# Optimization experiments

Measured on AMD Instinct MI355X. Metric: run time of the kernel, lower is better.

## Reference

```python
import jax, jax.numpy as jnp
import numpy as np

B, F, Hh, Ww, C = 1, 8, 12, 18, 1920
HEADS, HD, RANK, TXT = 30, 64, 128, 224
VID = F * Hh * Ww  # 1728
DN = ('NCH', 'OIH', 'NCH')


def setup_inputs() -> dict:
    key = jax.random.key(0)
    ks = jax.random.split(key, 14)
    s = 0.02
    return {
        'hidden_states': jax.random.normal(ks[0], (B, VID, C), jnp.float32),
        'encoder_hidden_states': jax.random.normal(ks[1], (B, TXT, C), jnp.float32),
        'cos': jax.random.uniform(ks[2], (VID, HD), jnp.float32),
        'sin': jax.random.uniform(ks[3], (VID, HD), jnp.float32),
        'conv1_w': jax.random.normal(ks[4], (RANK, C, 3), jnp.float32) * s,
        'conv2_w': jax.random.normal(ks[5], (C, RANK, 3), jnp.float32) * s,
        'Wq': jax.random.normal(ks[6], (C, C), jnp.float32) * s,
        'bq': jnp.zeros((C,), jnp.float32),
        'Wk': jax.random.normal(ks[7], (C, C), jnp.float32) * s,
        'bk': jnp.zeros((C,), jnp.float32),
        'Wv': jax.random.normal(ks[8], (C, C), jnp.float32) * s,
        'bv': jnp.zeros((C,), jnp.float32),
        'Wo': jax.random.normal(ks[9], (C, C), jnp.float32) * s,
        'bo': jnp.zeros((C,), jnp.float32),
    }


def _rope(x, cos, sin):
    # x: [B, H, S_vid, D]; cos/sin: [S_vid, D]; interleaved rotate-half
    xr = x.reshape(*x.shape[:-1], -1, 2)
    x_rot = jnp.stack([-xr[..., 1], xr[..., 0]], axis=-1).reshape(x.shape)
    return x * cos + x_rot * sin


def reference(hidden_states, encoder_hidden_states, cos, sin, conv1_w, conv2_w,
              Wq, bq, Wk, bk, Wv, bv, Wo, bo):
    # temporal conv1d skip branch over frame axis per spatial location
    x = hidden_states.reshape(B, F, Hh, Ww, C).transpose(0, 2, 3, 4, 1)
    x = x.reshape(B * Hh * Ww, C, F)
    h = jax.lax.conv_general_dilated(x, conv1_w, (1,), [(1, 1)], dimension_numbers=DN)
    h = jax.nn.gelu(h, approximate=False)
    h = jax.lax.conv_general_dilated(h, conv2_w, (1,), [(1, 1)], dimension_numbers=DN)
    skip = h.reshape(B, Hh, Ww, C, F).transpose(0, 4, 1, 2, 3).reshape(B, VID, C)

    hs = jnp.concatenate([encoder_hidden_states, hidden_states + skip], axis=1)  # [B,S,C]

    q = (hs @ Wq.T + bq).reshape(B, -1, HEADS, HD).transpose(0, 2, 1, 3)
    k = (hs @ Wk.T + bk).reshape(B, -1, HEADS, HD).transpose(0, 2, 1, 3)
    v = (hs @ Wv.T + bv).reshape(B, -1, HEADS, HD).transpose(0, 2, 1, 3)

    # RoPE applied only to the video (image) tokens of q and k
    q = jnp.concatenate([q[:, :, :TXT], _rope(q[:, :, TXT:], cos, sin)], axis=2)
    k = jnp.concatenate([k[:, :, :TXT], _rope(k[:, :, TXT:], cos, sin)], axis=2)

    scores = jnp.einsum('bhqd,bhkd->bhqk', q, k) * (HD ** -0.5)
    attn = jax.nn.softmax(scores, axis=-1)
    o = jnp.einsum('bhqk,bhkd->bhqd', attn, v)
    o = o.transpose(0, 2, 1, 3).reshape(B, -1, HEADS * HD)
    o = o @ Wo.T + bo  # to_out[0]; to_out[1] is dropout (identity at eval)

    return (o[:, TXT:], o[:, :TXT])  # (hidden_states, encoder_hidden_states)
```

## Files before the change

### kernel.cpp

```cpp
#include <hip/hip_runtime.h>
#include <math.h>

typedef unsigned short u16;
typedef short short8 __attribute__((ext_vector_type(8)));
typedef short shortv4 __attribute__((ext_vector_type(4)));
typedef float f32x4 __attribute__((ext_vector_type(4)));

#define TXT 224
#define VID 1728
#define S_ALL 1952
#define C_DIM 1920
#define HD 64
#define RANK 128
#define SHD 124928

#define OFF_HS   ((size_t)0)
#define OFF_XPAD ((size_t)3932160)
#define OFF_O    OFF_XPAD
#define OFF_HG   ((size_t)8355840)
#define OFF_W1T  ((size_t)8650752)
#define OFF_W2T  ((size_t)9388032)
#define OFF_WQ   ((size_t)10125312)
#define OFF_WK   ((size_t)13811712)
#define OFF_WV   ((size_t)17498112)
#define OFF_WO   ((size_t)21184512)
#define OFF_Q    ((size_t)24870912)
#define OFF_K    ((size_t)28618752)
#define OFF_V    ((size_t)32366592)

__device__ __forceinline__ float b2f(u16 u) {
  union { unsigned int i; float f; } x; x.i = ((unsigned int)u) << 16; return x.f;
}
__device__ __forceinline__ u16 f2b(float f) {
  union { float f; unsigned int i; } x; x.f = f;
  unsigned int i = x.i;
  return (u16)((i + 0x7FFFu + ((i >> 16) & 1u)) >> 16);
}
__device__ __forceinline__ void gload16(const u16* g, short* l) {
  __builtin_amdgcn_global_load_lds((const __attribute__((address_space(1))) unsigned int*)g,
                                   (__attribute__((address_space(3))) unsigned int*)l, 16, 0, 0);
}

__global__ void __launch_bounds__(256) prep_kernel(const float* __restrict__ hidden,
                                                   const float* __restrict__ enc,
                                                   const float* __restrict__ w1,
                                                   const float* __restrict__ w2,
                                                   const float* __restrict__ Wq,
                                                   const float* __restrict__ Wk,
                                                   const float* __restrict__ Wv,
                                                   const float* __restrict__ Wo,
                                                   u16* __restrict__ ws) {
  size_t i = (size_t)blockIdx.x * 256 + threadIdx.x;
  if (i < 1105920) {
    const size_t e = i * 4;
    const int row = (int)(e / 1920), col = (int)(e % 1920);
    shortv4 o4 = {0, 0, 0, 0};
    if (row >= 216 && row < 1944) {
      const float4 f = *(const float4*)(hidden + (size_t)(row - 216) * 1920 + col);
      o4 = (shortv4){(short)f2b(f.x), (short)f2b(f.y), (short)f2b(f.z), (short)f2b(f.w)};
    }
    *(shortv4*)(ws + OFF_XPAD + e) = o4;
    return;
  }
  i -= 1105920;
  if (i < 184320) {
    const size_t e = i * 4;
    const int r = (int)(e / 5760), j = (int)(e % 5760), t = j / 1920, c = j % 1920;
    const float* s = w1 + (size_t)r * 5760 + (size_t)c * 3 + t;
    shortv4 o4 = {(short)f2b(s[0]), (short)f2b(s[3]), (short)f2b(s[6]), (short)f2b(s[9])};
    *(shortv4*)(ws + OFF_W1T + e) = o4;
    return;
  }
  i -= 184320;
  if (i < 184320) {
    const size_t e = i * 4;
    const int c = (int)(e / 384), j = (int)(e % 384), t = j / 128, r = j % 128;
    const float* s = w2 + (size_t)c * 384 + (size_t)r * 3 + t;
    shortv4 o4 = {(short)f2b(s[0]), (short)f2b(s[3]), (short)f2b(s[6]), (short)f2b(s[9])};
    *(shortv4*)(ws + OFF_W2T + e) = o4;
    return;
  }
  i -= 184320;
  if (i < 107520) {
    const size_t e = i * 4;
    const float4 f = *(const float4*)(enc + e);
    *(shortv4*)(ws + OFF_HS + e) =
        (shortv4){(short)f2b(f.x), (short)f2b(f.y), (short)f2b(f.z), (short)f2b(f.w)};
    return;
  }
  i -= 107520;
  if (i < 3686400) {
    const int j = (int)(i / 921600);
    const size_t e = (i - (size_t)j * 921600) * 4;
    const float* src = (j == 0) ? Wq : ((j == 1) ? Wk : ((j == 2) ? Wv : Wo));
    const float4 f = *(const float4*)(src + e);
    *(shortv4*)(ws + OFF_WQ + (size_t)j * 3686400 + e) =
        (shortv4){(short)f2b(f.x), (short)f2b(f.y), (short)f2b(f.z), (short)f2b(f.w)};
    return;
  }
  i -= 3686400;
  const short8 z8 = {0, 0, 0, 0, 0, 0, 0, 0};
  size_t e;
  if (i < 23040) e = OFF_HS + 3747840 + i * 8;
  else if (i < 26496) e = OFF_HG + (i - 23040) * 8;
  else if (i < 32256) e = OFF_HG + 248832 + (i - 26496) * 8;
  else e = OFF_O + 3747840 + (i - 32256) * 8;
  *(short8*)(ws + e) = z8;
}

struct GArgs {
  const u16 *A, *B0, *B1, *B2;
  const float *bias0, *bias1, *bias2;
  const float *cosp, *sinp, *hidden;
  u16 *out0, *out1, *out2;
  float* outf;
  int lda, ldb, ksteps, spt, tap_rows, nMt, nNt, Mvalid;
};

template <int BM, int BN, int EPI>
__global__ void __launch_bounds__(256) gemm_bt(GArgs a) {
  constexpr int WM = BM / 2, WN = BN / 2, FM = WM / 16, FN = WN / 16;
  __shared__ __align__(16) short lA[2][BM * 32];
  __shared__ __align__(16) short lB[2][BN * 32];
  const int tid = threadIdx.x;
  const int lane = tid & 63;
  const int wv = tid >> 6, wr = wv >> 1, wc = wv & 1;
  const int lr = lane & 15, lg = lane >> 4;
  const int mtile = blockIdx.x % a.nMt;
  const int ntile_raw = blockIdx.x / a.nMt;
  const int ntile = ntile_raw % a.nNt;
  const int slice = ntile_raw / a.nNt;
  const int kstart = slice * a.ksteps;
  const int sec = (ntile * BN) / C_DIM;
  const u16* Bw = (sec == 0) ? a.B0 : ((sec == 1) ? a.B1 : a.B2);
  const int nb = ntile * BN - sec * C_DIM;
  const int m0 = mtile * BM;

  f32x4 acc[FM][FN];
#pragma unroll
  for (int i = 0; i < FM; ++i)
#pragma unroll
    for (int j = 0; j < FN; ++j) acc[i][j] = (f32x4){0.f, 0.f, 0.f, 0.f};

  auto stageStep = [&](int buf, int gs) {
    const int tap = gs / a.spt;
    const int kcol = (gs - tap * a.spt) * 32;
    const int arow0 = m0 + tap * a.tap_rows;
#pragma unroll
    for (int i = 0; i < BM / 64; ++i) {
      const int o = (i * 256 + tid) * 16;
      const int row = o >> 6;
      const int ke = (o & 63) >> 1;
      gload16(a.A + (size_t)(arow0 + row) * a.lda + (kcol + ke), &lA[buf][o >> 1]);
    }
#pragma unroll
    for (int i = 0; i < BN / 64; ++i) {
      const int o = (i * 256 + tid) * 16;
      const int row = o >> 6;
      const int ke = (o & 63) >> 1;
      gload16(Bw + (size_t)(nb + row) * a.ldb + (gs * 32 + ke), &lB[buf][o >> 1]);
    }
  };

  stageStep(0, kstart);
  __syncthreads();
  int cur = 0;
  for (int s = 0; s < a.ksteps; ++s) {
    if (s + 1 < a.ksteps) stageStep(cur ^ 1, kstart + s + 1);
    short8 af[FM], bfr[FN];
#pragma unroll
    for (int i = 0; i < FM; ++i)
      af[i] = *(const short8*)(&lA[cur][(wr * WM + i * 16 + lr) * 32 + lg * 8]);
#pragma unroll
    for (int j = 0; j < FN; ++j)
      bfr[j] = *(const short8*)(&lB[cur][(wc * WN + j * 16 + lr) * 32 + lg * 8]);
#pragma unroll
    for (int i = 0; i < FM; ++i)
#pragma unroll
      for (int j = 0; j < FN; ++j)
        acc[i][j] = __builtin_amdgcn_mfma_f32_16x16x32_bf16(af[i], bfr[j], acc[i][j], 0, 0, 0);
    __syncthreads();
    cur ^= 1;
  }

#pragma unroll
  for (int i = 0; i < FM; ++i) {
#pragma unroll
    for (int j = 0; j < FN; ++j) {
      const int col = ntile * BN + wc * WN + j * 16 + lr;
#pragma unroll
      for (int r = 0; r < 4; ++r) {
        const int m = m0 + wr * WM + i * 16 + lg * 4 + r;
        float v = acc[i][j][r];
        if (EPI == 4) {
          if (m < a.Mvalid) a.outf[(size_t)slice * 221184 + (size_t)m * RANK + col] = v;
        } else if (EPI == 1) {
          if (m < a.Mvalid) {
            v += a.hidden[(size_t)m * C_DIM + col];
            a.out0[(size_t)m * C_DIM + col] = f2b(v);
          }
        } else if (EPI == 2) {
          const int nn = col - sec * C_DIM;
          const int hh = nn >> 6, d = nn & 63;
          const float* bias = (sec == 0) ? a.bias0 : ((sec == 1) ? a.bias1 : a.bias2);
          v += bias[nn];
          const float vp = __shfl_xor(v, 1);
          if (sec < 2 && m >= TXT) {
            const int vid = ((m < S_ALL) ? m : TXT) - TXT;
            const float c = a.cosp[vid * HD + d];
            const float sn = a.sinp[vid * HD + d];
            v = (d & 1) ? (v * c + vp * sn) : (v * c - vp * sn);
          }
          if (sec == 0) v *= 0.18033688011112042f;
          if (m < a.Mvalid) {
            u16* dst = (sec == 0) ? a.out0 : ((sec == 1) ? a.out1 : a.out2);
            dst[(size_t)hh * SHD + (size_t)m * HD + d] = f2b(v);
          }
        } else {
          v += a.bias0[col];
          if (m < a.Mvalid) {
            const int dr = (m >= TXT) ? (m - TXT) : (VID + m);
            a.outf[(size_t)dr * C_DIM + col] = v;
          }
        }
      }
    }
  }
}

__global__ void __launch_bounds__(256) c1reduce_kernel(const float* __restrict__ part,
                                                       u16* __restrict__ hg) {
  const int i = blockIdx.x * 256 + threadIdx.x;
  float s = 0.f;
#pragma unroll
  for (int j = 0; j < 6; ++j) s += part[(size_t)j * 221184 + i];
  const float g = 0.5f * s * (1.0f + erff(s * 0.70710678f));
  hg[i] = f2b(g);
}

__global__ void __launch_bounds__(256) vtrans_kernel(const u16* __restrict__ vin,
                                                     u16* __restrict__ vout) {
  __shared__ u16 t[64][72];
  const int b = blockIdx.x, hh = b / 31, mt = b % 31;
  const int m0 = mt * 64;
  const int rows = (m0 + 64 <= S_ALL) ? 64 : (S_ALL - m0);
  const int tid = threadIdx.x;
  const u16* src = vin + (size_t)hh * SHD + (size_t)m0 * HD;
#pragma unroll
  for (int p = 0; p < 2; ++p) {
    const int r = p * 32 + (tid >> 3), c = (tid & 7) * 8;
    short8 v8 = {0, 0, 0, 0, 0, 0, 0, 0};
    if (r < rows) v8 = *(const short8*)(src + (size_t)r * HD + c);
    *(short8*)&t[r][c] = v8;
  }
  __syncthreads();
  const int d = tid & 63, ms = tid >> 6;
  if (ms * 16 < rows) {
    short8 a0, a1;
#pragma unroll
    for (int x = 0; x < 8; ++x) { a0[x] = (short)t[ms * 16 + x][d]; a1[x] = (short)t[ms * 16 + 8 + x][d]; }
    u16* dst = vout + (size_t)hh * SHD + (size_t)d * S_ALL + m0 + ms * 16;
    *(short8*)dst = a0;
    *(short8*)(dst + 8) = a1;
  }
}

__global__ void __launch_bounds__(256) attn_kernel(const u16* __restrict__ q,
                                                   const u16* __restrict__ k,
                                                   const u16* __restrict__ vT,
                                                   u16* __restrict__ o) {
  __shared__ __align__(16) short lK[2][4096];
  __shared__ __align__(16) short lp[4][1024];
  const int bid = blockIdx.x;
  const int hh = bid / 31, qt = bid - hh * 31;
  const int tid = threadIdx.x, wv = tid >> 6, lane = tid & 63;
  const int lr = lane & 15, lg = lane >> 4;
  const int qbase = qt * 64 + wv * 16;
  const bool active = qbase < S_ALL;
  const u16* qh = q + (size_t)hh * SHD;
  const u16* kh = k + (size_t)hh * SHD;
  const u16* vh = vT + (size_t)hh * SHD;

  int krow[2], kcol[2], kdst[2];
#pragma unroll
  for (int j = 0; j < 2; ++j) {
    const int p0 = (j * 256 + tid) * 8;
    const int row = p0 >> 6, cs = p0 & 63;
    kdst[j] = p0;
    krow[j] = row;
    kcol[j] = cs ^ ((row & 7) * 8);
  }

  short8 aq0 = {}, aq1 = {};
  if (active) {
    aq0 = *(const short8*)(qh + (size_t)(qbase + lr) * HD + lg * 8);
    aq1 = *(const short8*)(qh + (size_t)(qbase + lr) * HD + 32 + lg * 8);
  }
  f32x4 oa[4];
#pragma unroll
  for (int gd = 0; gd < 4; ++gd) oa[gd] = (f32x4){0.f, 0.f, 0.f, 0.f};
  float mr = -3.0e38f, lw = 0.f;
  const f32x4 z4 = (f32x4){0.f, 0.f, 0.f, 0.f};
  const int pmask = (lr & 7) * 8;
  short* lpw = &lp[wv][0];
  const u16* vrow[4];
#pragma unroll
  for (int gd = 0; gd < 4; ++gd) vrow[gd] = vh + (size_t)(gd * 16 + lr) * S_ALL + lg * 8;

#pragma unroll
  for (int j = 0; j < 2; ++j) gload16(kh + (size_t)krow[j] * HD + kcol[j], &lK[0][kdst[j]]);
  __syncthreads();

  int cur = 0;
  for (int t = 0; t < 30; ++t) {
    const int kb = t * 64;
    if (t < 29) {
#pragma unroll
      for (int j = 0; j < 2; ++j)
        gload16(kh + (size_t)(kb + 64 + krow[j]) * HD + kcol[j], &lK[cur ^ 1][kdst[j]]);
    }
    if (active) {
      const short* Kt = &lK[cur][0];
      f32x4 st[4];
      __builtin_amdgcn_s_setprio(1);
#pragma unroll
      for (int k16 = 0; k16 < 4; ++k16) {
        const int row = k16 * 16 + lr;
        const int m8 = (row & 7) * 8;
        short8 kf0 = *(const short8*)(Kt + row * 64 + ((lg * 8) ^ m8));
        short8 kf1 = *(const short8*)(Kt + row * 64 + ((32 + lg * 8) ^ m8));
        st[k16] = __builtin_amdgcn_mfma_f32_16x16x32_bf16(kf0, aq0, z4, 0, 0, 0);
        st[k16] = __builtin_amdgcn_mfma_f32_16x16x32_bf16(kf1, aq1, st[k16], 0, 0, 0);
      }
      __builtin_amdgcn_s_setprio(0);
      short8 vf[4][2];
#pragma unroll
      for (int gd = 0; gd < 4; ++gd) {
        vf[gd][0] = *(const short8*)(vrow[gd] + kb);
        vf[gd][1] = *(const short8*)(vrow[gd] + kb + 32);
      }
      float tm = fmaxf(fmaxf(fmaxf(st[0][0], st[0][1]), fmaxf(st[0][2], st[0][3])),
                       fmaxf(fmaxf(st[1][0], st[1][1]), fmaxf(st[1][2], st[1][3])));
      tm = fmaxf(tm, fmaxf(fmaxf(fmaxf(st[2][0], st[2][1]), fmaxf(st[2][2], st[2][3])),
                           fmaxf(fmaxf(st[3][0], st[3][1]), fmaxf(st[3][2], st[3][3]))));
      tm = fmaxf(tm, __shfl_xor(tm, 16));
      tm = fmaxf(tm, __shfl_xor(tm, 32));
      const bool defer = (__all(tm <= mr + 8.0f) != 0);
      float al = 1.0f;
      if (!defer) {
        const float mn = fmaxf(mr, tm);
        al = __builtin_exp2f(mr - mn);
        mr = mn;
      }
      float rs = 0.f;
#pragma unroll
      for (int k16 = 0; k16 < 4; ++k16) {
        float p0 = __builtin_exp2f(st[k16][0] - mr);
        float p1 = __builtin_exp2f(st[k16][1] - mr);
        float p2 = __builtin_exp2f(st[k16][2] - mr);
        float p3 = __builtin_exp2f(st[k16][3] - mr);
        rs += (p0 + p1) + (p2 + p3);
        uint2 pk;
        asm("v_cvt_pk_bf16_f32 %0, %1, %2" : "=v"(pk.x) : "v"(p0), "v"(p1));
        asm("v_cvt_pk_bf16_f32 %0, %1, %2" : "=v"(pk.y) : "v"(p2), "v"(p3));
        *(uint2*)(lpw + lr * 64 + ((k16 * 16 + lg * 4) ^ pmask)) = pk;
      }
      rs += __shfl_xor(rs, 16);
      rs += __shfl_xor(rs, 32);
      lw = lw * al + rs;
      asm volatile("s_waitcnt lgkmcnt(0)" ::: "memory");
      short8 pa0 = *(const short8*)(lpw + lr * 64 + ((lg * 8) ^ pmask));
      short8 pa1 = *(const short8*)(lpw + lr * 64 + ((32 + lg * 8) ^ pmask));
      float alp[4];
      if (!defer) {
#pragma unroll
        for (int r = 0; r < 4; ++r) alp[r] = __shfl(al, lg * 4 + r);
      }
      __builtin_amdgcn_s_setprio(1);
#pragma unroll
      for (int gd = 0; gd < 4; ++gd) {
        f32x4 tacc = oa[gd];
        if (!defer) {
#pragma unroll
          for (int r = 0; r < 4; ++r) tacc[r] *= alp[r];
        }
        tacc = __builtin_amdgcn_mfma_f32_16x16x32_bf16(pa0, vf[gd][0], tacc, 0, 0, 0);
        oa[gd] = __builtin_amdgcn_mfma_f32_16x16x32_bf16(pa1, vf[gd][1], tacc, 0, 0, 0);
      }
      __builtin_amdgcn_s_setprio(0);
    }
    __syncthreads();
    cur ^= 1;
  }

  if (active) {
    const u16* kp = kh + (size_t)1920 * HD + (size_t)lr * HD + lg * 8;
    short8 kf00 = *(const short8*)(kp);
    short8 kf01 = *(const short8*)(kp + 32);
    short8 kf10 = *(const short8*)(kp + 16 * HD);
    short8 kf11 = *(const short8*)(kp + 16 * HD + 32);
    f32x4 st0 = __builtin_amdgcn_mfma_f32_16x16x32_bf16(kf00, aq0, z4, 0, 0, 0);
    st0 = __builtin_amdgcn_mfma_f32_16x16x32_bf16(kf01, aq1, st0, 0, 0, 0);
    f32x4 st1 = __builtin_amdgcn_mfma_f32_16x16x32_bf16(kf10, aq0, z4, 0, 0, 0);
    st1 = __builtin_amdgcn_mfma_f32_16x16x32_bf16(kf11, aq1, st1, 0, 0, 0);
    float tm = fmaxf(fmaxf(fmaxf(st0[0], st0[1]), fmaxf(st0[2], st0[3])),
                     fmaxf(fmaxf(st1[0], st1[1]), fmaxf(st1[2], st1[3])));
    tm = fmaxf(tm, __shfl_xor(tm, 16));
    tm = fmaxf(tm, __shfl_xor(tm, 32));
    const float mn = fmaxf(mr, tm);
    const float al = __builtin_exp2f(mr - mn);
    mr = mn;
    float rs = 0.f;
    float pp[8];
#pragma unroll
    for (int r = 0; r < 4; ++r) { pp[r] = __builtin_exp2f(st0[r] - mn); rs += pp[r]; }
#pragma unroll
    for (int r = 0; r < 4; ++r) { pp[4 + r] = __builtin_exp2f(st1[r] - mn); rs += pp[4 + r]; }
    {
      uint2 pk;
      asm("v_cvt_pk_bf16_f32 %0, %1, %2" : "=v"(pk.x) : "v"(pp[0]), "v"(pp[1]));
      asm("v_cvt_pk_bf16_f32 %0, %1, %2" : "=v"(pk.y) : "v"(pp[2]), "v"(pp[3]));
      *(uint2*)(lpw + lr * 64 + ((lg * 4) ^ pmask)) = pk;
      asm("v_cvt_pk_bf16_f32 %0, %1, %2" : "=v"(pk.x) : "v"(pp[4]), "v"(pp[5]));
      asm("v_cvt_pk_bf16_f32 %0, %1, %2" : "=v"(pk.y) : "v"(pp[6]), "v"(pp[7]));
      *(uint2*)(lpw + lr * 64 + ((16 + lg * 4) ^ pmask)) = pk;
    }
    rs += __shfl_xor(rs, 16);
    rs += __shfl_xor(rs, 32);
    lw = lw * al + rs;
    asm volatile("s_waitcnt lgkmcnt(0)" ::: "memory");
    short8 pa0 = *(const short8*)(lpw + lr * 64 + ((lg * 8) ^ pmask));
    float alp[4];
#pragma unroll
    for (int r = 0; r < 4; ++r) alp[r] = __shfl(al, lg * 4 + r);
#pragma unroll
    for (int gd = 0; gd < 4; ++gd) {
      short8 vf = *(const short8*)(vrow[gd] + 1920);
      f32x4 tacc = oa[gd];
#pragma unroll
      for (int r = 0; r < 4; ++r) tacc[r] *= alp[r];
      oa[gd] = __builtin_amdgcn_mfma_f32_16x16x32_bf16(pa0, vf, tacc, 0, 0, 0);
    }
    float lwp[4];
#pragma unroll
    for (int r = 0; r < 4; ++r) lwp[r] = 1.0f / __shfl(lw, lg * 4 + r);
#pragma unroll
    for (int gd = 0; gd < 4; ++gd) {
      const int col = hh * HD + gd * 16 + lr;
#pragma unroll
      for (int r = 0; r < 4; ++r) {
        const int m = qbase + lg * 4 + r;
        o[(size_t)m * C_DIM + col] = f2b(oa[gd][r] * lwp[r]);
      }
    }
  }
}

extern "C" void kernel_launch(void* const* d_in, const int* in_sizes, int n_in,
                              void* d_out, int out_size, void* d_ws, size_t ws_size,
                              hipStream_t stream) {
  const float* hidden = (const float*)d_in[0];
  const float* enc = (const float*)d_in[1];
  const float* cosp = (const float*)d_in[2];
  const float* sinp = (const float*)d_in[3];
  const float* w1 = (const float*)d_in[4];
  const float* w2 = (const float*)d_in[5];
  const float* bq = (const float*)d_in[7];
  const float* bk = (const float*)d_in[9];
  const float* bv = (const float*)d_in[11];
  const float* bo = (const float*)d_in[13];
  u16* ws = (u16*)d_ws;
  float* out = (float*)d_out;

  prep_kernel<<<20796, 256, 0, stream>>>(hidden, enc, w1, w2, (const float*)d_in[6],
                                         (const float*)d_in[8], (const float*)d_in[10],
                                         (const float*)d_in[12], ws);

  GArgs c1{};
  c1.A = ws + OFF_XPAD; c1.B0 = c1.B1 = c1.B2 = ws + OFF_W1T;
  c1.lda = C_DIM; c1.ldb = 5760; c1.ksteps = 30; c1.spt = 60; c1.tap_rows = 216;
  c1.nMt = 27; c1.nNt = 2; c1.Mvalid = VID;
  c1.outf = (float*)(ws + OFF_Q);
  gemm_bt<64, 64, 4><<<324, 256, 0, stream>>>(c1);

  c1reduce_kernel<<<864, 256, 0, stream>>>((const float*)(ws + OFF_Q),
                                           ws + OFF_HG + (size_t)216 * RANK);

  GArgs c2{};
  c2.A = ws + OFF_HG; c2.B0 = c2.B1 = c2.B2 = ws + OFF_W2T;
  c2.lda = RANK; c2.ldb = 384; c2.ksteps = 12; c2.spt = 4; c2.tap_rows = 216;
  c2.nMt = 14; c2.nNt = 15; c2.Mvalid = VID; c2.hidden = hidden;
  c2.out0 = ws + OFF_HS + (size_t)TXT * C_DIM;
  gemm_bt<128, 128, 1><<<210, 256, 0, stream>>>(c2);

  GArgs c3{};
  c3.A = ws + OFF_HS; c3.B0 = ws + OFF_WQ; c3.B1 = ws + OFF_WK; c3.B2 = ws + OFF_WV;
  c3.bias0 = bq; c3.bias1 = bk; c3.bias2 = bv; c3.cosp = cosp; c3.sinp = sinp;
  c3.lda = C_DIM; c3.ldb = C_DIM; c3.ksteps = 60; c3.spt = 60; c3.tap_rows = 0;
  c3.nMt = 16; c3.nNt = 45; c3.Mvalid = S_ALL;
  c3.out0 = ws + OFF_Q; c3.out1 = ws + OFF_K; c3.out2 = ws + OFF_O;
  gemm_bt<128, 128, 2><<<720, 256, 0, stream>>>(c3);

  vtrans_kernel<<<930, 256, 0, stream>>>(ws + OFF_O, ws + OFF_V);

  attn_kernel<<<930, 256, 0, stream>>>(ws + OFF_Q, ws + OFF_K, ws + OFF_V, ws + OFF_O);

  GArgs c4{};
  c4.A = ws + OFF_O; c4.B0 = c4.B1 = c4.B2 = ws + OFF_WO; c4.bias0 = bo;
  c4.lda = C_DIM; c4.ldb = C_DIM; c4.ksteps = 60; c4.spt = 60; c4.tap_rows = 0;
  c4.nMt = 32; c4.nNt = 15; c4.Mvalid = S_ALL;
  c4.outf = out;
  gemm_bt<64, 128, 3><<<480, 256, 0, stream>>>(c4);
}
```

Before: 299.2 us.

## Stage V tiles in LDS and compute softmax row sums with MFMA

V tiles are now double-buffered into shared memory alongside K using the same swizzled async loads, instead of being read per-wave from global memory each iteration. The softmax row sum is computed by an MFMA against a ones vector on the bf16 P tile, which removes the scalar adds and cross-lane shuffles. The max reduction is also reshaped into a flatter tree. This costs extra LDS (another 16 KB), which may lower occupancy, and the row sum now comes from bf16-rounded probabilities.

Result: faster. 278.0 us (-7.1%).

```diff
diff --git a/kernel.cpp b/kernel.cpp
--- a/kernel.cpp
+++ b/kernel.cpp
@@ -270,6 +270,7 @@
                                                    const u16* __restrict__ vT,
                                                    u16* __restrict__ o) {
   __shared__ __align__(16) short lK[2][4096];
+  __shared__ __align__(16) short lV[2][4096];
   __shared__ __align__(16) short lp[4][1024];
   const int bid = blockIdx.x;
   const int hh = bid / 31, qt = bid - hh * 31;
@@ -299,16 +300,17 @@
   f32x4 oa[4];
 #pragma unroll
   for (int gd = 0; gd < 4; ++gd) oa[gd] = (f32x4){0.f, 0.f, 0.f, 0.f};
-  float mr = -3.0e38f, lw = 0.f;
+  float mr = -3.0e38f;
+  float lw_pv[4] = {0.f, 0.f, 0.f, 0.f};
   const f32x4 z4 = (f32x4){0.f, 0.f, 0.f, 0.f};
+  const short8 onesb = {16256, 16256, 16256, 16256, 16256, 16256, 16256, 16256};
   const int pmask = (lr & 7) * 8;
   short* lpw = &lp[wv][0];
-  const u16* vrow[4];
-#pragma unroll
-  for (int gd = 0; gd < 4; ++gd) vrow[gd] = vh + (size_t)(gd * 16 + lr) * S_ALL + lg * 8;
 
 #pragma unroll
   for (int j = 0; j < 2; ++j) gload16(kh + (size_t)krow[j] * HD + kcol[j], &lK[0][kdst[j]]);
+#pragma unroll
+  for (int j = 0; j < 2; ++j) gload16(vh + (size_t)krow[j] * S_ALL + kcol[j], &lV[0][kdst[j]]);
   __syncthreads();
 
   int cur = 0;
@@ -318,9 +320,13 @@
 #pragma unroll
       for (int j = 0; j < 2; ++j)
         gload16(kh + (size_t)(kb + 64 + krow[j]) * HD + kcol[j], &lK[cur ^ 1][kdst[j]]);
+#pragma unroll
+      for (int j = 0; j < 2; ++j)
+        gload16(vh + (size_t)krow[j] * S_ALL + (kb + 64 + kcol[j]), &lV[cur ^ 1][kdst[j]]);
     }
     if (active) {
       const short* Kt = &lK[cur][0];
+      const short* Vt = &lV[cur][0];
       f32x4 st[4];
       __builtin_amdgcn_s_setprio(1);
 #pragma unroll
@@ -336,13 +342,19 @@
       short8 vf[4][2];
 #pragma unroll
       for (int gd = 0; gd < 4; ++gd) {
-        vf[gd][0] = *(const short8*)(vrow[gd] + kb);
-        vf[gd][1] = *(const short8*)(vrow[gd] + kb + 32);
-      }
-      float tm = fmaxf(fmaxf(fmaxf(st[0][0], st[0][1]), fmaxf(st[0][2], st[0][3])),
-                       fmaxf(fmaxf(st[1][0], st[1][1]), fmaxf(st[1][2], st[1][3])));
-      tm = fmaxf(tm, fmaxf(fmaxf(fmaxf(st[2][0], st[2][1]), fmaxf(st[2][2], st[2][3])),
-                           fmaxf(fmaxf(st[3][0], st[3][1]), fmaxf(st[3][2], st[3][3]))));
+        const int row = gd * 16 + lr;
+        const int m8 = (row & 7) * 8;
+        vf[gd][0] = *(const short8*)(Vt + row * 64 + ((lg * 8) ^ m8));
+        vf[gd][1] = *(const short8*)(Vt + row * 64 + ((32 + lg * 8) ^ m8));
+      }
+      float ta = fmaxf(fmaxf(st[0][0], st[0][1]), st[0][2]);
+      float tb = fmaxf(fmaxf(st[0][3], st[1][0]), st[1][1]);
+      float tc = fmaxf(fmaxf(st[1][2], st[1][3]), st[2][0]);
+      float td = fmaxf(fmaxf(st[2][1], st[2][2]), st[2][3]);
+      float te = fmaxf(fmaxf(st[3][0], st[3][1]), st[3][2]);
+      float tm = fmaxf(fmaxf(ta, tb), tc);
+      tm = fmaxf(fmaxf(tm, td), te);
+      tm = fmaxf(tm, st[3][3]);
       tm = fmaxf(tm, __shfl_xor(tm, 16));
       tm = fmaxf(tm, __shfl_xor(tm, 32));
       const bool defer = (__all(tm <= mr + 8.0f) != 0);
@@ -352,22 +364,17 @@
         al = __builtin_exp2f(mr - mn);
         mr = mn;
       }
-      float rs = 0.f;
 #pragma unroll
       for (int k16 = 0; k16 < 4; ++k16) {
         float p0 = __builtin_exp2f(st[k16][0] - mr);
         float p1 = __builtin_exp2f(st[k16][1] - mr);
         float p2 = __builtin_exp2f(st[k16][2] - mr);
         float p3 = __builtin_exp2f(st[k16][3] - mr);
-        rs += (p0 + p1) + (p2 + p3);
         uint2 pk;
         asm("v_cvt_pk_bf16_f32 %0, %1, %2" : "=v"(pk.x) : "v"(p0), "v"(p1));
         asm("v_cvt_pk_bf16_f32 %0, %1, %2" : "=v"(pk.y) : "v"(p2), "v"(p3));
         *(uint2*)(lpw + lr * 64 + ((k16 * 16 + lg * 4) ^ pmask)) = pk;
       }
-      rs += __shfl_xor(rs, 16);
-      rs += __shfl_xor(rs, 32);
-      lw = lw * al + rs;
       asm volatile("s_waitcnt lgkmcnt(0)" ::: "memory");
       short8 pa0 = *(const short8*)(lpw + lr * 64 + ((lg * 8) ^ pmask));
       short8 pa1 = *(const short8*)(lpw + lr * 64 + ((32 + lg * 8) ^ pmask));
@@ -377,6 +384,15 @@
         for (int r = 0; r < 4; ++r) alp[r] = __shfl(al, lg * 4 + r);
       }
       __builtin_amdgcn_s_setprio(1);
+      f32x4 rsum = __builtin_amdgcn_mfma_f32_16x16x32_bf16(pa0, onesb, z4, 0, 0, 0);
+      rsum = __builtin_amdgcn_mfma_f32_16x16x32_bf16(pa1, onesb, rsum, 0, 0, 0);
+      if (defer) {
+#pragma unroll
+        for (int r = 0; r < 4; ++r) lw_pv[r] += rsum[r];
+      } else {
+#pragma unroll
+        for (int r = 0; r < 4; ++r) lw_pv[r] = lw_pv[r] * alp[r] + rsum[r];
+      }
 #pragma unroll
       for (int gd = 0; gd < 4; ++gd) {
         f32x4 tacc = oa[gd];
@@ -403,19 +419,18 @@
     st0 = __builtin_amdgcn_mfma_f32_16x16x32_bf16(kf01, aq1, st0, 0, 0, 0);
     f32x4 st1 = __builtin_amdgcn_mfma_f32_16x16x32_bf16(kf10, aq0, z4, 0, 0, 0);
     st1 = __builtin_amdgcn_mfma_f32_16x16x32_bf16(kf11, aq1, st1, 0, 0, 0);
-    float tm = fmaxf(fmaxf(fmaxf(st0[0], st0[1]), fmaxf(st0[2], st0[3])),
-                     fmaxf(fmaxf(st1[0], st1[1]), fmaxf(st1[2], st1[3])));
+    float ta = fmaxf(fmaxf(st0[0], st0[1]), st0[2]);
+    float tb = fmaxf(fmaxf(st0[3], st1[0]), st1[1]);
+    float tm = fmaxf(fmaxf(ta, tb), fmaxf(st1[2], st1[3]));
     tm = fmaxf(tm, __shfl_xor(tm, 16));
     tm = fmaxf(tm, __shfl_xor(tm, 32));
     const float mn = fmaxf(mr, tm);
     const float al = __builtin_exp2f(mr - mn);
-    mr = mn;
-    float rs = 0.f;
     float pp[8];
 #pragma unroll
-    for (int r = 0; r < 4; ++r) { pp[r] = __builtin_exp2f(st0[r] - mn); rs += pp[r]; }
-#pragma unroll
-    for (int r = 0; r < 4; ++r) { pp[4 + r] = __builtin_exp2f(st1[r] - mn); rs += pp[4 + r]; }
+    for (int r = 0; r < 4; ++r) pp[r] = __builtin_exp2f(st0[r] - mn);
+#pragma unroll
+    for (int r = 0; r < 4; ++r) pp[4 + r] = __builtin_exp2f(st1[r] - mn);
     {
       uint2 pk;
       asm("v_cvt_pk_bf16_f32 %0, %1, %2" : "=v"(pk.x) : "v"(pp[0]), "v"(pp[1]));
@@ -425,17 +440,17 @@
       asm("v_cvt_pk_bf16_f32 %0, %1, %2" : "=v"(pk.y) : "v"(pp[6]), "v"(pp[7]));
       *(uint2*)(lpw + lr * 64 + ((16 + lg * 4) ^ pmask)) = pk;
     }
-    rs += __shfl_xor(rs, 16);
-    rs += __shfl_xor(rs, 32);
-    lw = lw * al + rs;
     asm volatile("s_waitcnt lgkmcnt(0)" ::: "memory");
     short8 pa0 = *(const short8*)(lpw + lr * 64 + ((lg * 8) ^ pmask));
     float alp[4];
 #pragma unroll
     for (int r = 0; r < 4; ++r) alp[r] = __shfl(al, lg * 4 + r);
+    f32x4 rsum = __builtin_amdgcn_mfma_f32_16x16x32_bf16(pa0, onesb, z4, 0, 0, 0);
+#pragma unroll
+    for (int r = 0; r < 4; ++r) lw_pv[r] = lw_pv[r] * alp[r] + rsum[r];
 #pragma unroll
     for (int gd = 0; gd < 4; ++gd) {
-      short8 vf = *(const short8*)(vrow[gd] + 1920);
+      short8 vf = *(const short8*)(vh + (size_t)(gd * 16 + lr) * S_ALL + 1920 + lg * 8);
       f32x4 tacc = oa[gd];
 #pragma unroll
       for (int r = 0; r < 4; ++r) tacc[r] *= alp[r];
@@ -443,7 +458,7 @@
     }
     float lwp[4];
 #pragma unroll
-    for (int r = 0; r < 4; ++r) lwp[r] = 1.0f / __shfl(lw, lg * 4 + r);
+    for (int r = 0; r < 4; ++r) lwp[r] = 1.0f / lw_pv[r];
 #pragma unroll
     for (int gd = 0; gd < 4; ++gd) {
       const int col = hh * HD + gd * 16 + lr;
```
